# Optimization experiments

Measured on AMD Instinct MI355X. Metric: run time of the kernel, lower is better.

## Reference

```python
import jax, jax.numpy as jnp
import numpy as np

N_NODES = 80000
N_EDGES = 1280000
IN_CH = 128
HID = 64
N_GRAPHS = 64
DROPOUT_P = 0.3


def setup_inputs() -> dict:
    key = jax.random.key(0)
    ks = jax.random.split(key, 12)
    x = jax.random.normal(ks[0], (N_NODES, IN_CH), dtype=jnp.float32)
    edge_index = jax.random.randint(ks[1], (2, N_EDGES), 0, N_NODES, dtype=jnp.int64 if jax.config.read('jax_enable_x64') else jnp.int32)
    batch = jnp.sort(jax.random.randint(ks[2], (N_NODES,), 0, N_GRAPHS))
    def lin(k, fan_in, fan_out):
        lim = 1.0 / np.sqrt(fan_in)
        kw, kb = jax.random.split(k)
        W = jax.random.uniform(kw, (fan_in, fan_out), minval=-lim, maxval=lim, dtype=jnp.float32)
        b = jax.random.uniform(kb, (fan_out,), minval=-lim, maxval=lim, dtype=jnp.float32)
        return W, b
    W1, b1 = lin(ks[3], IN_CH, HID)
    W2, b2 = lin(ks[4], HID, HID)
    W3, b3 = lin(ks[5], HID, HID)
    Wm1, bm1 = lin(ks[6], HID, HID)
    Wm2, bm2 = lin(ks[7], HID, 1)
    return {"x": x, "edge_index": edge_index, "batch": batch,
            "W1": W1, "b1": b1, "W2": W2, "b2": b2, "W3": W3, "b3": b3,
            "Wm1": Wm1, "bm1": bm1, "Wm2": Wm2, "bm2": bm2}


def _gcn_conv(x, W, b, src, dst, deg_inv_sqrt):
    # PyG GCNConv: h = X W; add self-loops; norm_e = d^-1/2[src] * d^-1/2[dst]
    h = x @ W  # [N, F]
    norm = deg_inv_sqrt[src] * deg_inv_sqrt[dst]  # [E]
    agg = jax.ops.segment_sum(h[src] * norm[:, None], dst, num_segments=x.shape[0])
    agg = agg + h * (deg_inv_sqrt * deg_inv_sqrt)[:, None]  # self-loop term d^-1
    return agg + b


def _dropout(x, key, p):
    keep = jax.random.bernoulli(key, 1.0 - p, x.shape)
    return jnp.where(keep, x / (1.0 - p), 0.0)


def reference(x, edge_index, batch, W1, b1, W2, b2, W3, b3, Wm1, bm1, Wm2, bm2):
    src, dst = edge_index[0], edge_index[1]
    N = x.shape[0]
    # in-degree on dst, +1 for self-loop (PyG default normalization)
    deg = jax.ops.segment_sum(jnp.ones_like(dst, dtype=x.dtype), dst, num_segments=N) + 1.0
    deg_inv_sqrt = jax.lax.rsqrt(deg)

    dk = jax.random.split(jax.random.key(42), 4)
    h = _dropout(jax.nn.relu(_gcn_conv(x, W1, b1, src, dst, deg_inv_sqrt)), dk[0], DROPOUT_P)
    h = _dropout(jax.nn.relu(_gcn_conv(h, W2, b2, src, dst, deg_inv_sqrt)), dk[1], DROPOUT_P)
    h = _dropout(jax.nn.relu(_gcn_conv(h, W3, b3, src, dst, deg_inv_sqrt)), dk[2], DROPOUT_P)

    # global mean pool per graph
    sums = jax.ops.segment_sum(h, batch, num_segments=N_GRAPHS)
    counts = jax.ops.segment_sum(jnp.ones((N,), dtype=h.dtype), batch, num_segments=N_GRAPHS)
    pooled = sums / jnp.maximum(counts, 1.0)[:, None]  # [G, HID]

    # MLP head: Linear -> ReLU -> Dropout -> Linear
    m = jax.nn.relu(pooled @ Wm1 + bm1)
    m = _dropout(m, dk[3], DROPOUT_P)
    return m @ Wm2 + bm2  # [G, 1]
```

## Files before the change

### kernel.cpp

```cpp
#include <hip/hip_runtime.h>
#include <hip/hip_fp8.h>
#include <stdint.h>

#define HID 64
#define INCH 128
#define NGRAPH 64
#define KEEPP 0.7f
#define CAP 64
#define CAPSH 6
#define BD 16
#define CPAD 4

typedef __attribute__((ext_vector_type(8))) short short8;
typedef __attribute__((ext_vector_type(4))) float floatx4;

__device__ __forceinline__ uint8_t f2e4(float f) {
  __hip_fp8_e4m3 t(f);
  return (uint8_t)t.__x;
}
__device__ __forceinline__ float e42f(uint8_t b) {
  __hip_fp8_e4m3 t;
  t.__x = (__hip_fp8_storage_t)b;
  return (float)t;
}
__device__ __forceinline__ ushort f2bf(float v) {
  uint32_t u = __float_as_uint(v);
  return (ushort)((u + 0x7FFFu + ((u >> 16) & 1u)) >> 16);
}
__device__ __forceinline__ float bf2f(ushort b) {
  return __uint_as_float((uint32_t)b << 16);
}

__host__ __device__ inline void tf2x32(uint32_t k0, uint32_t k1,
                                       uint32_t& x0, uint32_t& x1) {
  const uint32_t ks2 = k0 ^ k1 ^ 0x1BD11BDAu;
#define ROTL32(v, d) (((v) << (d)) | ((v) >> (32 - (d))))
#define TF_RND(r) { x0 += x1; x1 = ROTL32(x1, r); x1 ^= x0; }
  x0 += k0; x1 += k1;
  TF_RND(13) TF_RND(15) TF_RND(26) TF_RND(6)
  x0 += k1;  x1 += ks2 + 1u;
  TF_RND(17) TF_RND(29) TF_RND(16) TF_RND(24)
  x0 += ks2; x1 += k0 + 2u;
  TF_RND(13) TF_RND(15) TF_RND(26) TF_RND(6)
  x0 += k0;  x1 += k1 + 3u;
  TF_RND(17) TF_RND(29) TF_RND(16) TF_RND(24)
  x0 += k1;  x1 += ks2 + 4u;
  TF_RND(13) TF_RND(15) TF_RND(26) TF_RND(6)
  x0 += ks2; x1 += k0 + 5u;
#undef TF_RND
#undef ROTL32
}

__device__ __forceinline__ bool keep_mask(uint32_t k0, uint32_t k1, uint32_t idx) {
  uint32_t x0 = 0u, x1 = idx;
  tf2x32(k0, k1, x0, x1);
  uint32_t bits = x0 ^ x1;
  float u = __uint_as_float((bits >> 9) | 0x3f800000u) - 1.0f;
  return u < KEEPP;
}

__device__ __forceinline__ void wsplit_one(const float* __restrict__ W,
                                           short8* __restrict__ Wh,
                                           short8* __restrict__ Wl, int i) {
  int lane = i & 63, f = i >> 6;
  int kc = f >> 2, ct = f & 3;
  int kbase = kc * 32 + ((lane >> 4) << 3);
  int n = ct * 16 + (lane & 15);
  short8 h, l;
#pragma unroll
  for (int j = 0; j < 8; ++j) {
    float w = W[(size_t)(kbase + j) * HID + n];
    uint32_t u = __float_as_uint(w);
    h[j] = (short)(u >> 16);
    float r = w - __uint_as_float(u & 0xFFFF0000u);
    l[j] = (short)(__float_as_uint(r) >> 16);
  }
  Wh[i] = h;
  Wl[i] = l;
}

__global__ __launch_bounds__(256) void k_w1(const float* __restrict__ W1,
                                            short8* __restrict__ Wh1,
                                            short8* __restrict__ Wl1) {
  wsplit_one(W1, Wh1, Wl1, blockIdx.x * 256 + (int)threadIdx.x);
}

template <int K>
__device__ __forceinline__ void mgemm_tile_f32(const float* __restrict__ A,
                                               const short8* __restrict__ Wh,
                                               const short8* __restrict__ Wl,
                                               ushort* __restrict__ C,
                                               int N, int tile) {
  constexpr int KC = K / 32;
  const int lane = threadIdx.x & 63;
  const int wv = threadIdx.x >> 6;
  const int m = lane & 15;
  const int q = lane >> 4;
  const int row0 = tile * 64 + wv * 16;
  if (row0 >= N) return;
  const int arow = min(row0 + m, N - 1);
  const float* __restrict__ ap = A + (size_t)arow * K + (q << 3);

  floatx4 acc[4];
#pragma unroll
  for (int ct = 0; ct < 4; ++ct) acc[ct] = (floatx4){0.f, 0.f, 0.f, 0.f};

#pragma unroll
  for (int kc = 0; kc < KC; ++kc) {
    const floatx4* apv = (const floatx4*)(ap + kc * 32);
    floatx4 x0 = apv[0];
    floatx4 x1 = apv[1];
    short8 ah, al;
#pragma unroll
    for (int j = 0; j < 4; ++j) {
      uint32_t u = __float_as_uint(x0[j]);
      ah[j] = (short)(u >> 16);
      float r = x0[j] - __uint_as_float(u & 0xFFFF0000u);
      al[j] = (short)(__float_as_uint(r) >> 16);
    }
#pragma unroll
    for (int j = 0; j < 4; ++j) {
      uint32_t u = __float_as_uint(x1[j]);
      ah[4 + j] = (short)(u >> 16);
      float r = x1[j] - __uint_as_float(u & 0xFFFF0000u);
      al[4 + j] = (short)(__float_as_uint(r) >> 16);
    }
#pragma unroll
    for (int ct = 0; ct < 4; ++ct) {
      short8 bh = Wh[(kc * 4 + ct) * 64 + lane];
      short8 bl = Wl[(kc * 4 + ct) * 64 + lane];
      acc[ct] = __builtin_amdgcn_mfma_f32_16x16x32_bf16(ah, bh, acc[ct], 0, 0, 0);
      acc[ct] = __builtin_amdgcn_mfma_f32_16x16x32_bf16(ah, bl, acc[ct], 0, 0, 0);
      acc[ct] = __builtin_amdgcn_mfma_f32_16x16x32_bf16(al, bh, acc[ct], 0, 0, 0);
    }
  }

  ushort* __restrict__ cp = C + (size_t)row0 * HID;
#pragma unroll
  for (int ct = 0; ct < 4; ++ct)
#pragma unroll
    for (int r = 0; r < 4; ++r) {
      int rr = (q << 2) + r;
      if (row0 + rr < N) cp[(size_t)rr * HID + ct * 16 + m] = f2bf(acc[ct][r]);
    }
}

template <int K>
__global__ __launch_bounds__(256) void k_build_gemm(
    const float* __restrict__ A, const short8* __restrict__ Wh,
    const short8* __restrict__ Wl, ushort* __restrict__ C, int N,
    const int* __restrict__ src, const int* __restrict__ dst,
    int* __restrict__ counts, int* __restrict__ cap,
    int E, int build_blocks, int gemm_blocks,
    const float* __restrict__ W2, short8* __restrict__ Wh2, short8* __restrict__ Wl2,
    const float* __restrict__ W3, short8* __restrict__ Wh3, short8* __restrict__ Wl3,
    const int* __restrict__ batch, int* __restrict__ gends) {
  const int TB = build_blocks + gemm_blocks;
  const int tid = (int)threadIdx.x;
  if ((int)blockIdx.x >= TB) {
    int xb = (int)blockIdx.x - TB;
    if (xb < 2) {
      wsplit_one(W2, Wh2, Wl2, xb * 256 + tid);
    } else if (xb < 4) {
      wsplit_one(W3, Wh3, Wl3, (xb - 2) * 256 + tid);
    } else {
      int bi = xb - 4;
      for (int i = bi * 256 + tid; i < N; i += BD * 256) {
        int g = batch[i];
        int gn = (i + 1 < N) ? batch[i + 1] : -1;
        if (g != gn) gends[g] = i + 1;
      }
    }
    return;
  }
  const long T = (long)TB;
  const long b = (long)blockIdx.x;
  const long gb = (b * gemm_blocks) / T;
  const bool is_g = (((b + 1) * gemm_blocks) / T) != gb;
  if (!is_g) {
    int bb = (int)(b - gb);
    int e = bb * 256 + tid;
    if (e < E) {
      int s = src[e], d = dst[e];
      int r = atomicAdd(&counts[d << CPAD], 1);
      if (r < CAP) cap[(d << CAPSH) + r] = s;
    }
    return;
  }
  mgemm_tile_f32<K>(A, Wh, Wl, C, N, (int)gb);
}

template <int K>
__global__ __launch_bounds__(256) void k_mgemm_b(const ushort* __restrict__ A,
                                                 const short8* __restrict__ Wh,
                                                 const short8* __restrict__ Wl,
                                                 uint8_t* __restrict__ C,
                                                 const int* __restrict__ counts,
                                                 int N) {
  constexpr int KC = K / 32;
  const int lane = threadIdx.x & 63;
  const int wv = threadIdx.x >> 6;
  const int m = lane & 15;
  const int q = lane >> 4;
  const int row0 = (int)blockIdx.x * 64 + wv * 16;
  if (row0 >= N) return;
  const int arow = min(row0 + m, N - 1);
  const ushort* __restrict__ ap = A + (size_t)arow * K + (q << 3);

  floatx4 acc[4];
#pragma unroll
  for (int ct = 0; ct < 4; ++ct) acc[ct] = (floatx4){0.f, 0.f, 0.f, 0.f};

#pragma unroll
  for (int kc = 0; kc < KC; ++kc) {
    short8 ah = *(const short8*)(ap + kc * 32);
#pragma unroll
    for (int ct = 0; ct < 4; ++ct) {
      short8 bh = Wh[(kc * 4 + ct) * 64 + lane];
      short8 bl = Wl[(kc * 4 + ct) * 64 + lane];
      acc[ct] = __builtin_amdgcn_mfma_f32_16x16x32_bf16(ah, bh, acc[ct], 0, 0, 0);
      acc[ct] = __builtin_amdgcn_mfma_f32_16x16x32_bf16(ah, bl, acc[ct], 0, 0, 0);
    }
  }

  float dv[4];
#pragma unroll
  for (int r = 0; r < 4; ++r) {
    int gr = min(row0 + (q << 2) + r, N - 1);
    dv[r] = rsqrtf((float)counts[gr << CPAD] + 1.0f);
  }
  uint8_t* __restrict__ cp = C + (size_t)row0 * HID;
#pragma unroll
  for (int ct = 0; ct < 4; ++ct)
#pragma unroll
    for (int r = 0; r < 4; ++r) {
      int rr = (q << 2) + r;
      if (row0 + rr < N) cp[(size_t)rr * HID + ct * 16 + m] = f2e4(acc[ct][r] * dv[r]);
    }
}

__global__ __launch_bounds__(256) void k_scale(const ushort* __restrict__ Bh,
                                               const int* __restrict__ counts,
                                               uint8_t* __restrict__ B0, int N) {
  int t = blockIdx.x * 256 + threadIdx.x;
  int total = N * (HID / 8);
  if (t >= total) return;
  int node = t >> 3;
  float dn = rsqrtf((float)counts[node << CPAD] + 1.0f);
  const ushort* ip = Bh + (size_t)t * 8;
  ushort4 a = *(const ushort4*)ip;
  ushort4 b = *(const ushort4*)(ip + 4);
  uint8_t o[8];
  o[0] = f2e4(bf2f(a.x) * dn); o[1] = f2e4(bf2f(a.y) * dn);
  o[2] = f2e4(bf2f(a.z) * dn); o[3] = f2e4(bf2f(a.w) * dn);
  o[4] = f2e4(bf2f(b.x) * dn); o[5] = f2e4(bf2f(b.y) * dn);
  o[6] = f2e4(bf2f(b.z) * dn); o[7] = f2e4(bf2f(b.w) * dn);
  *(uint2*)(B0 + (size_t)t * 8) = *(uint2*)o;
}

__global__ __launch_bounds__(256) void k_gather_s(const uint8_t* __restrict__ tmp,
                                                  const int* __restrict__ counts,
                                                  const int* __restrict__ cap,
                                                  const float* __restrict__ bias,
                                                  ushort* __restrict__ outh, int N,
                                                  uint32_t k0, uint32_t k1) {
  const int node = blockIdx.x * 4 + (threadIdx.x >> 6);
  const int lane = threadIdx.x & 63;
  if (node >= N) return;
  const int degn = __builtin_amdgcn_readfirstlane(counts[node << CPAD]);
  const int deg = min(degn, CAP);
  const int base = node << CAPSH;
  const int idx = node * HID + lane;
  const float selfv = e42f(tmp[idx]);
  const float blane = bias[lane];
  const int sub = lane >> 4;
  const int ch4 = (lane & 15) << 2;
  float a0 = 0.0f, a1 = 0.0f, a2 = 0.0f, a3 = 0.0f;
  for (int j = 0; j < deg; j += 8) {
    int4 ea = *(const int4*)&cap[base + j];
    int4 eb = *(const int4*)&cap[base + j + 4];
    int sa = (sub & 1) ? ea.y : ea.x;
    int ta = (sub & 1) ? ea.w : ea.z;
    sa = (sub & 2) ? ta : sa;
    int sb = (sub & 1) ? eb.y : eb.x;
    int tb = (sub & 1) ? eb.w : eb.z;
    sb = (sub & 2) ? tb : sb;
    uint32_t wa = 0u, wb = 0u;
    if (j + sub < deg)
      wa = *(const uint32_t*)(tmp + ((size_t)sa << 6) + ch4);
    if (j + 4 + sub < deg)
      wb = *(const uint32_t*)(tmp + ((size_t)sb << 6) + ch4);
    a0 += e42f((uint8_t)(wa & 255u));
    a1 += e42f((uint8_t)((wa >> 8) & 255u));
    a2 += e42f((uint8_t)((wa >> 16) & 255u));
    a3 += e42f((uint8_t)(wa >> 24));
    a0 += e42f((uint8_t)(wb & 255u));
    a1 += e42f((uint8_t)((wb >> 8) & 255u));
    a2 += e42f((uint8_t)((wb >> 16) & 255u));
    a3 += e42f((uint8_t)(wb >> 24));
  }
  a0 += __shfl_xor(a0, 16); a1 += __shfl_xor(a1, 16);
  a2 += __shfl_xor(a2, 16); a3 += __shfl_xor(a3, 16);
  a0 += __shfl_xor(a0, 32); a1 += __shfl_xor(a1, 32);
  a2 += __shfl_xor(a2, 32); a3 += __shfl_xor(a3, 32);
  const int srcl = lane >> 2;
  float t0 = __shfl(a0, srcl);
  float t1 = __shfl(a1, srcl);
  float t2 = __shfl(a2, srcl);
  float t3 = __shfl(a3, srcl);
  float u01 = (lane & 1) ? t1 : t0;
  float u23 = (lane & 1) ? t3 : t2;
  float acc = (lane & 2) ? u23 : u01;

  const float dn = rsqrtf((float)degn + 1.0f);
  float v = dn * (acc + selfv) + blane;
  v = fmaxf(v, 0.0f);
  v = keep_mask(k0, k1, (uint32_t)idx) ? v / KEEPP : 0.0f;
  outh[idx] = f2bf(v);
}

__global__ __launch_bounds__(256) void k_pool(const ushort* __restrict__ h,
                                              const int* __restrict__ batch,
                                              float* __restrict__ sums, int N) {
  __shared__ float ls[NGRAPH * HID];
  for (int i = threadIdx.x; i < NGRAPH * HID; i += 256) ls[i] = 0.0f;
  __syncthreads();
  const int lane = threadIdx.x & 63;
  const int wave = threadIdx.x >> 6;
  int per = (N + gridDim.x - 1) / gridDim.x;
  int beg = blockIdx.x * per;
  int end = min(N, beg + per);
  for (int i = beg + wave; i < end; i += 4) {
    int g = batch[i];
    atomicAdd(&ls[g * HID + lane], bf2f(h[(size_t)i * HID + lane]));
  }
  __syncthreads();
  for (int i = threadIdx.x; i < NGRAPH * HID; i += 256)
    if (ls[i] != 0.0f) atomicAdd(&sums[i], ls[i]);
}

__global__ __launch_bounds__(256) void k_head(const float* __restrict__ sums,
                                              const int* __restrict__ gends,
                                              const float* __restrict__ Wm1,
                                              const float* __restrict__ bm1,
                                              const float* __restrict__ Wm2,
                                              const float* __restrict__ bm2,
                                              float* __restrict__ out,
                                              uint32_t k0, uint32_t k1) {
  __shared__ float cnts_s[NGRAPH];
  __shared__ float pooled[NGRAPH * HID];
  __shared__ float m[NGRAPH * HID];
  if (threadIdx.x < 64) {
    int g = threadIdx.x;
    int e = gends[g];
#pragma unroll
    for (int off = 1; off < 64; off <<= 1) {
      int o = __shfl_up(e, off);
      if (g >= off) e = max(e, o);
    }
    int prev = __shfl_up(e, 1);
    if (g == 0) prev = 0;
    cnts_s[g] = (float)(e - prev);
  }
  __syncthreads();
  for (int i = threadIdx.x; i < NGRAPH * HID; i += 256) {
    int g = i >> 6;
    pooled[i] = sums[i] / fmaxf(cnts_s[g], 1.0f);
  }
  __syncthreads();
  for (int i = threadIdx.x; i < NGRAPH * HID; i += 256) {
    int g = i >> 6, j = i & 63;
    float acc = bm1[j];
#pragma unroll 8
    for (int k = 0; k < HID; ++k)
      acc = fmaf(pooled[g * HID + k], Wm1[k * HID + j], acc);
    acc = fmaxf(acc, 0.0f);
    m[i] = keep_mask(k0, k1, (uint32_t)i) ? acc / KEEPP : 0.0f;
  }
  __syncthreads();
  if (threadIdx.x < NGRAPH) {
    int g = threadIdx.x;
    float acc = bm2[0];
#pragma unroll 8
    for (int j = 0; j < HID; ++j)
      acc = fmaf(m[g * HID + j], Wm2[j], acc);
    out[g] = acc;
  }
}

extern "C" void kernel_launch(void* const* d_in, const int* in_sizes, int n_in,
                              void* d_out, int out_size, void* d_ws, size_t ws_size,
                              hipStream_t stream) {
  const float* x     = (const float*)d_in[0];
  const int*   ei    = (const int*)d_in[1];
  const int*   batch = (const int*)d_in[2];
  const float* W1 = (const float*)d_in[3];
  const float* b1 = (const float*)d_in[4];
  const float* W2 = (const float*)d_in[5];
  const float* b2 = (const float*)d_in[6];
  const float* W3 = (const float*)d_in[7];
  const float* b3 = (const float*)d_in[8];
  const float* Wm1 = (const float*)d_in[9];
  const float* bm1 = (const float*)d_in[10];
  const float* Wm2 = (const float*)d_in[11];
  const float* bm2 = (const float*)d_in[12];
  float* out = (float*)d_out;

  const int N = in_sizes[0] / INCH;
  const int E = in_sizes[1] / 2;
  const int* src = ei;
  const int* dst = ei + E;

  char* ws = (char*)d_ws;
  size_t off = 0;
  uint8_t* B0 = (uint8_t*)(ws + off); off += (size_t)N * HID;
  off = (off + 63) & ~(size_t)63;
  ushort* B1    = (ushort*)(ws + off); off += (size_t)N * HID * 2;
  off = (off + 63) & ~(size_t)63;
  int*   counts = (int*)  (ws + off); off += ((size_t)N << CPAD) * 4;
  float* sums   = (float*)(ws + off); off += NGRAPH * HID * 4;
  int*   gends  = (int*)  (ws + off); off += NGRAPH * 4;
  int*   cap    = (int*)  (ws + off); off += (size_t)N * CAP * 4;
  off = (off + 15) & ~(size_t)15;
  short8* Wh1 = (short8*)(ws + off); off += 1024 * 16;
  short8* Wl1 = (short8*)(ws + off); off += 1024 * 16;
  short8* Wh2 = (short8*)(ws + off); off += 512 * 16;
  short8* Wl2 = (short8*)(ws + off); off += 512 * 16;
  short8* Wh3 = (short8*)(ws + off); off += 512 * 16;
  short8* Wl3 = (short8*)(ws + off); off += 512 * 16;
  ushort* Bh = B1;

  uint32_t dk[4][2];
  for (uint32_t i = 0; i < 4; ++i) {
    uint32_t a = 0u, b = i;
    tf2x32(0u, 42u, a, b);
    dk[i][0] = a; dk[i][1] = b;
  }

  const int build_grid = (E + 255) / 256;
  const int mg_grid    = (N + 63) / 64;
  const int gath_grid  = (N + 3) / 4;
  const int scale_grid = (N * (HID / 8) + 255) / 256;

  hipMemsetAsync(counts, 0,
                 ((size_t)N << CPAD) * 4 + NGRAPH * HID * 4 + NGRAPH * 4, stream);
  k_w1<<<4, 256, 0, stream>>>(W1, Wh1, Wl1);

  k_build_gemm<INCH><<<build_grid + mg_grid + 4 + BD, 256, 0, stream>>>(
      x, Wh1, Wl1, Bh, N, src, dst, counts, cap, E,
      build_grid, mg_grid, W2, Wh2, Wl2, W3, Wh3, Wl3, batch, gends);
  k_scale<<<scale_grid, 256, 0, stream>>>(Bh, counts, B0, N);
  k_gather_s<<<gath_grid, 256, 0, stream>>>(B0, counts, cap, b1,
                                            B1, N, dk[0][0], dk[0][1]);
  k_mgemm_b<HID><<<mg_grid, 256, 0, stream>>>(B1, Wh2, Wl2, B0, counts, N);
  k_gather_s<<<gath_grid, 256, 0, stream>>>(B0, counts, cap, b2,
                                            B1, N, dk[1][0], dk[1][1]);
  k_mgemm_b<HID><<<mg_grid, 256, 0, stream>>>(B1, Wh3, Wl3, B0, counts, N);
  k_gather_s<<<gath_grid, 256, 0, stream>>>(B0, counts, cap, b3,
                                            B1, N, dk[2][0], dk[2][1]);

  k_pool<<<256, 256, 0, stream>>>(B1, batch, sums, N);
  k_head<<<1, 256, 0, stream>>>(sums, gends, Wm1, bm1, Wm2, bm2, out,
                                dk[3][0], dk[3][1]);
  (void)n_in; (void)out_size; (void)ws_size;
}
```

Before: 369.4 us.

## Split neighbor gather into two source-range passes for cache locality

Edges are bucketed by whether the source node falls in the lower or upper half of the node range. Low-half sources fill the adjacency slots from the front and high-half sources from the back, each with its own counter. Each aggregation then runs as two kernels, one per source half, so each pass touches only half the feature table and is more likely to stay cache-resident. The cost is an extra launch per layer, a bf16 partial-sum buffer written and read between the passes, and an extra rounding step. The per-node counters also become unpadded, so build atomics on them may contend more.

```diff
diff --git a/kernel.cpp b/kernel.cpp
--- a/kernel.cpp
+++ b/kernel.cpp
@@ -9,7 +9,6 @@
 #define CAP 64
 #define CAPSH 6
 #define BD 16
-#define CPAD 4
 
 typedef __attribute__((ext_vector_type(8))) short short8;
 typedef __attribute__((ext_vector_type(4))) float floatx4;
@@ -150,8 +149,8 @@
     const float* __restrict__ A, const short8* __restrict__ Wh,
     const short8* __restrict__ Wl, ushort* __restrict__ C, int N,
     const int* __restrict__ src, const int* __restrict__ dst,
-    int* __restrict__ counts, int* __restrict__ cap,
-    int E, int build_blocks, int gemm_blocks,
+    int* __restrict__ clo, int* __restrict__ chi, int* __restrict__ cap,
+    int E, int build_blocks, int gemm_blocks, int half,
     const float* __restrict__ W2, short8* __restrict__ Wh2, short8* __restrict__ Wl2,
     const float* __restrict__ W3, short8* __restrict__ Wh3, short8* __restrict__ Wl3,
     const int* __restrict__ batch, int* __restrict__ gends) {
@@ -182,8 +181,13 @@
     int e = bb * 256 + tid;
     if (e < E) {
       int s = src[e], d = dst[e];
-      int r = atomicAdd(&counts[d << CPAD], 1);
-      if (r < CAP) cap[(d << CAPSH) + r] = s;
+      if (s < half) {
+        int r = atomicAdd(&clo[d], 1);
+        if (r < CAP) cap[(d << CAPSH) + r] = s;
+      } else {
+        int r = atomicAdd(&chi[d], 1);
+        if (r < CAP) cap[(d << CAPSH) + (CAP - 1 - r)] = s;
+      }
     }
     return;
   }
@@ -195,7 +199,8 @@
                                                  const short8* __restrict__ Wh,
                                                  const short8* __restrict__ Wl,
                                                  uint8_t* __restrict__ C,
-                                                 const int* __restrict__ counts,
+                                                 const int* __restrict__ clo,
+                                                 const int* __restrict__ chi,
                                                  int N) {
   constexpr int KC = K / 32;
   const int lane = threadIdx.x & 63;
@@ -227,7 +232,7 @@
 #pragma unroll
   for (int r = 0; r < 4; ++r) {
     int gr = min(row0 + (q << 2) + r, N - 1);
-    dv[r] = rsqrtf((float)counts[gr << CPAD] + 1.0f);
+    dv[r] = rsqrtf((float)(clo[gr] + chi[gr]) + 1.0f);
   }
   uint8_t* __restrict__ cp = C + (size_t)row0 * HID;
 #pragma unroll
@@ -240,13 +245,14 @@
 }
 
 __global__ __launch_bounds__(256) void k_scale(const ushort* __restrict__ Bh,
-                                               const int* __restrict__ counts,
+                                               const int* __restrict__ clo,
+                                               const int* __restrict__ chi,
                                                uint8_t* __restrict__ B0, int N) {
   int t = blockIdx.x * 256 + threadIdx.x;
   int total = N * (HID / 8);
   if (t >= total) return;
   int node = t >> 3;
-  float dn = rsqrtf((float)counts[node << CPAD] + 1.0f);
+  float dn = rsqrtf((float)(clo[node] + chi[node]) + 1.0f);
   const ushort* ip = Bh + (size_t)t * 8;
   ushort4 a = *(const ushort4*)ip;
   ushort4 b = *(const ushort4*)(ip + 4);
@@ -258,25 +264,34 @@
   *(uint2*)(B0 + (size_t)t * 8) = *(uint2*)o;
 }
 
-__global__ __launch_bounds__(256) void k_gather_s(const uint8_t* __restrict__ tmp,
-                                                  const int* __restrict__ counts,
-                                                  const int* __restrict__ cap,
-                                                  const float* __restrict__ bias,
-                                                  ushort* __restrict__ outh, int N,
-                                                  uint32_t k0, uint32_t k1) {
+template <int PHASE>
+__global__ __launch_bounds__(256) void k_gather2(const uint8_t* __restrict__ tmp,
+                                                 const int* __restrict__ clo,
+                                                 const int* __restrict__ chi,
+                                                 const int* __restrict__ cap,
+                                                 const float* __restrict__ bias,
+                                                 const ushort* __restrict__ part,
+                                                 ushort* __restrict__ outw, int N,
+                                                 uint32_t k0, uint32_t k1) {
   const int node = blockIdx.x * 4 + (threadIdx.x >> 6);
   const int lane = threadIdx.x & 63;
   if (node >= N) return;
-  const int degn = __builtin_amdgcn_readfirstlane(counts[node << CPAD]);
-  const int deg = min(degn, CAP);
   const int base = node << CAPSH;
   const int idx = node * HID + lane;
-  const float selfv = e42f(tmp[idx]);
-  const float blane = bias[lane];
   const int sub = lane >> 4;
   const int ch4 = (lane & 15) << 2;
   float a0 = 0.0f, a1 = 0.0f, a2 = 0.0f, a3 = 0.0f;
-  for (int j = 0; j < deg; j += 8) {
+
+  int j0, j1, lim;
+  if (PHASE == 0) {
+    const int lo = min(__builtin_amdgcn_readfirstlane(clo[node]), CAP);
+    j0 = 0; j1 = lo; lim = -1;
+  } else {
+    const int hi = min(__builtin_amdgcn_readfirstlane(chi[node]), CAP);
+    lim = CAP - hi;
+    j0 = lim & ~7; j1 = (hi > 0) ? CAP : 0;
+  }
+  for (int j = j0; j < j1; j += 8) {
     int4 ea = *(const int4*)&cap[base + j];
     int4 eb = *(const int4*)&cap[base + j + 4];
     int sa = (sub & 1) ? ea.y : ea.x;
@@ -285,11 +300,12 @@
     int sb = (sub & 1) ? eb.y : eb.x;
     int tb = (sub & 1) ? eb.w : eb.z;
     sb = (sub & 2) ? tb : sb;
+    bool va, vb;
+    if (PHASE == 0) { va = (j + sub < j1);       vb = (j + 4 + sub < j1); }
+    else            { va = (j + sub >= lim);     vb = (j + 4 + sub >= lim); }
     uint32_t wa = 0u, wb = 0u;
-    if (j + sub < deg)
-      wa = *(const uint32_t*)(tmp + ((size_t)sa << 6) + ch4);
-    if (j + 4 + sub < deg)
-      wb = *(const uint32_t*)(tmp + ((size_t)sb << 6) + ch4);
+    if (va) wa = *(const uint32_t*)(tmp + ((size_t)sa << 6) + ch4);
+    if (vb) wb = *(const uint32_t*)(tmp + ((size_t)sb << 6) + ch4);
     a0 += e42f((uint8_t)(wa & 255u));
     a1 += e42f((uint8_t)((wa >> 8) & 255u));
     a2 += e42f((uint8_t)((wa >> 16) & 255u));
@@ -312,11 +328,18 @@
   float u23 = (lane & 1) ? t3 : t2;
   float acc = (lane & 2) ? u23 : u01;
 
-  const float dn = rsqrtf((float)degn + 1.0f);
-  float v = dn * (acc + selfv) + blane;
-  v = fmaxf(v, 0.0f);
-  v = keep_mask(k0, k1, (uint32_t)idx) ? v / KEEPP : 0.0f;
-  outh[idx] = f2bf(v);
+  if (PHASE == 0) {
+    outw[idx] = f2bf(acc);
+  } else {
+    acc += bf2f(part[idx]);
+    const int degn = __builtin_amdgcn_readfirstlane(clo[node]) +
+                     __builtin_amdgcn_readfirstlane(chi[node]);
+    const float dn = rsqrtf((float)degn + 1.0f);
+    float v = dn * (acc + e42f(tmp[idx])) + bias[lane];
+    v = fmaxf(v, 0.0f);
+    v = keep_mask(k0, k1, (uint32_t)idx) ? v / KEEPP : 0.0f;
+    outw[idx] = f2bf(v);
+  }
 }
 
 __global__ __launch_bounds__(256) void k_pool(const ushort* __restrict__ h,
@@ -408,6 +431,7 @@
 
   const int N = in_sizes[0] / INCH;
   const int E = in_sizes[1] / 2;
+  const int half = N / 2;
   const int* src = ei;
   const int* dst = ei + E;
 
@@ -417,7 +441,10 @@
   off = (off + 63) & ~(size_t)63;
   ushort* B1    = (ushort*)(ws + off); off += (size_t)N * HID * 2;
   off = (off + 63) & ~(size_t)63;
-  int*   counts = (int*)  (ws + off); off += ((size_t)N << CPAD) * 4;
+  ushort* Bp    = (ushort*)(ws + off); off += (size_t)N * HID * 2;
+  off = (off + 63) & ~(size_t)63;
+  int*   clo    = (int*)  (ws + off); off += (size_t)N * 4;
+  int*   chi    = (int*)  (ws + off); off += (size_t)N * 4;
   float* sums   = (float*)(ws + off); off += NGRAPH * HID * 4;
   int*   gends  = (int*)  (ws + off); off += NGRAPH * 4;
   int*   cap    = (int*)  (ws + off); off += (size_t)N * CAP * 4;
@@ -442,22 +469,29 @@
   const int gath_grid  = (N + 3) / 4;
   const int scale_grid = (N * (HID / 8) + 255) / 256;
 
-  hipMemsetAsync(counts, 0,
-                 ((size_t)N << CPAD) * 4 + NGRAPH * HID * 4 + NGRAPH * 4, stream);
+  hipMemsetAsync(clo, 0,
+                 (size_t)N * 8 + NGRAPH * HID * 4 + NGRAPH * 4, stream);
   k_w1<<<4, 256, 0, stream>>>(W1, Wh1, Wl1);
 
   k_build_gemm<INCH><<<build_grid + mg_grid + 4 + BD, 256, 0, stream>>>(
-      x, Wh1, Wl1, Bh, N, src, dst, counts, cap, E,
-      build_grid, mg_grid, W2, Wh2, Wl2, W3, Wh3, Wl3, batch, gends);
-  k_scale<<<scale_grid, 256, 0, stream>>>(Bh, counts, B0, N);
-  k_gather_s<<<gath_grid, 256, 0, stream>>>(B0, counts, cap, b1,
-                                            B1, N, dk[0][0], dk[0][1]);
-  k_mgemm_b<HID><<<mg_grid, 256, 0, stream>>>(B1, Wh2, Wl2, B0, counts, N);
-  k_gather_s<<<gath_grid, 256, 0, stream>>>(B0, counts, cap, b2,
-                                            B1, N, dk[1][0], dk[1][1]);
-  k_mgemm_b<HID><<<mg_grid, 256, 0, stream>>>(B1, Wh3, Wl3, B0, counts, N);
-  k_gather_s<<<gath_grid, 256, 0, stream>>>(B0, counts, cap, b3,
-                                            B1, N, dk[2][0], dk[2][1]);
+      x, Wh1, Wl1, Bh, N, src, dst, clo, chi, cap, E,
+      build_grid, mg_grid, half, W2, Wh2, Wl2, W3, Wh3, Wl3, batch, gends);
+  k_scale<<<scale_grid, 256, 0, stream>>>(Bh, clo, chi, B0, N);
+
+  k_gather2<0><<<gath_grid, 256, 0, stream>>>(B0, clo, chi, cap, b1, nullptr,
+                                              Bp, N, dk[0][0], dk[0][1]);
+  k_gather2<1><<<gath_grid, 256, 0, stream>>>(B0, clo, chi, cap, b1, Bp,
+                                              B1, N, dk[0][0], dk[0][1]);
+  k_mgemm_b<HID><<<mg_grid, 256, 0, stream>>>(B1, Wh2, Wl2, B0, clo, chi, N);
+  k_gather2<0><<<gath_grid, 256, 0, stream>>>(B0, clo, chi, cap, b2, nullptr,
+                                              Bp, N, dk[1][0], dk[1][1]);
+  k_gather2<1><<<gath_grid, 256, 0, stream>>>(B0, clo, chi, cap, b2, Bp,
+                                              B1, N, dk[1][0], dk[1][1]);
+  k_mgemm_b<HID><<<mg_grid, 256, 0, stream>>>(B1, Wh3, Wl3, B0, clo, chi, N);
+  k_gather2<0><<<gath_grid, 256, 0, stream>>>(B0, clo, chi, cap, b3, nullptr,
+                                              Bp, N, dk[2][0], dk[2][1]);
+  k_gather2<1><<<gath_grid, 256, 0, stream>>>(B0, clo, chi, cap, b3, Bp,
+                                              B1, N, dk[2][0], dk[2][1]);
 
   k_pool<<<256, 256, 0, stream>>>(B1, batch, sums, N);
   k_head<<<1, 256, 0, stream>>>(sums, gends, Wm1, bm1, Wm2, bm2, out,
```

Result: slower. 412.1 us (+11.6%).
